# Optimization experiments

Hardware: AMD Instinct MI355X
Metric: run time of the kernel (lower is better)

The kernel has to match this reference:

```python
import jax, jax.numpy as jnp
import numpy as np

N = 50000      # nodes
E = 1600000    # edges
H = 128        # hidden_dim
P = 28         # pocket_dim
G = 256        # graphs in the batch
EPS = 1e-5     # BatchNorm eps


def setup_inputs() -> dict:
    key = jax.random.key(0)
    ks = jax.random.split(key, 24)
    s = 0.05
    inp = {
        "x": jax.random.normal(ks[0], (N, 7), jnp.float32),
        "edge_index": jax.random.randint(ks[1], (2, E), 0, N, jnp.int64),
        "batch": jnp.sort(jax.random.randint(ks[2], (N,), 0, G, jnp.int64)),
        "pocket_features": jax.random.normal(ks[3], (P,), jnp.float32),
        # GCN conv weights (first layer 7->128, layers 2..3 stacked 128->128)
        "conv0_W": jax.random.normal(ks[4], (7, H), jnp.float32) * s,
        "conv0_b": jnp.zeros((H,), jnp.float32),
        "convs_W": jax.random.normal(ks[5], (2, H, H), jnp.float32) * s,
        "convs_b": jnp.zeros((2, H), jnp.float32),
        # BatchNorm (eval mode) params per layer, stacked [3, H]
        "bn_gamma": jnp.ones((3, H), jnp.float32),
        "bn_beta": jnp.zeros((3, H), jnp.float32),
        "bn_mean": jax.random.normal(ks[6], (3, H), jnp.float32) * 0.1,
        "bn_var": jax.random.uniform(ks[7], (3, H), jnp.float32, 0.5, 1.5),
        # pocket MLP 28->64->64
        "pmlp_W1": jax.random.normal(ks[8], (P, 64), jnp.float32) * s,
        "pmlp_b1": jnp.zeros((64,), jnp.float32),
        "pmlp_W2": jax.random.normal(ks[9], (64, 64), jnp.float32) * s,
        "pmlp_b2": jnp.zeros((64,), jnp.float32),
        # Bilinear: torch weight shape [out=64, in1=H, in2=64]
        "bil_W": jax.random.normal(ks[10], (64, H, 64), jnp.float32) * s,
        "bil_b": jnp.zeros((64,), jnp.float32),
        # classifier 64->32->1
        "cls_W1": jax.random.normal(ks[11], (64, 32), jnp.float32) * s,
        "cls_b1": jnp.zeros((32,), jnp.float32),
        "cls_W2": jax.random.normal(ks[12], (32, 1), jnp.float32) * s,
        "cls_b2": jnp.zeros((1,), jnp.float32),
    }
    return inp


def _gcn(x, W, b, src, dst, dinv):
    """PyG GCNConv: sym-normalized aggregation with added self loops."""
    h = x @ W                                  # [N, H']
    norm = dinv[src] * dinv[dst]               # [E]
    agg = jax.ops.segment_sum(norm[:, None] * h[src], dst, num_segments=N)
    agg = agg + (dinv * dinv)[:, None] * h     # self-loop contribution
    return agg + b


def reference(x, edge_index, batch, pocket_features,
              conv0_W, conv0_b, convs_W, convs_b,
              bn_gamma, bn_beta, bn_mean, bn_var,
              pmlp_W1, pmlp_b1, pmlp_W2, pmlp_b2,
              bil_W, bil_b, cls_W1, cls_b1, cls_W2, cls_b2):
    src, dst = edge_index[0], edge_index[1]
    # degree over targets, with +1 for the self loop
    deg = jax.ops.segment_sum(jnp.ones((E,), x.dtype), dst, num_segments=N) + 1.0
    dinv = jax.lax.rsqrt(deg)

    h = x
    for i in range(3):
        W = conv0_W if i == 0 else convs_W[i - 1]
        b = conv0_b if i == 0 else convs_b[i - 1]
        h = _gcn(h, W, b, src, dst, dinv)
        # BatchNorm1d in eval mode; dropout = identity in eval
        h = bn_gamma[i] * (h - bn_mean[i]) * jax.lax.rsqrt(bn_var[i] + EPS) + bn_beta[i]
        h = jax.nn.relu(h)

    # global_mean_pool over graph ids
    sums = jax.ops.segment_sum(h, batch, num_segments=G)              # [G, H]
    cnt = jax.ops.segment_sum(jnp.ones((N,), h.dtype), batch, num_segments=G)
    ligand = sums / jnp.maximum(cnt, 1.0)[:, None]                    # [G, H]

    pk = jax.nn.relu(pocket_features @ pmlp_W1 + pmlp_b1) @ pmlp_W2 + pmlp_b2  # [64]
    pk = jnp.broadcast_to(pk, (G, 64))

    inter = jnp.einsum('bi,oij,bj->bo', ligand, bil_W, pk) + bil_b    # [G, 64]
    z = jax.nn.relu(inter @ cls_W1 + cls_b1) @ cls_W2 + cls_b2        # [G, 1]
    return z[:, 0]
```

## Files before the change

### kernel.cpp

```cpp
#include <hip/hip_runtime.h>

#define EPSBN 1e-5f
#define BCAP 12288
#define OVCAP 262144
#define INS_CAP 24
#define INS_STRIDE 25

#if defined(__has_builtin)
#if __has_builtin(__builtin_amdgcn_cvt_pk_f32_fp8) && __has_builtin(__builtin_amdgcn_cvt_pk_fp8_f32)
#define HAS_CVT_FP8 1
#endif
#endif

typedef float v2f_t __attribute__((ext_vector_type(2)));
typedef __attribute__((ext_vector_type(8))) short bf16x8;
typedef __attribute__((ext_vector_type(4))) float f32x4;

__device__ inline unsigned short f2bf(float f) {
    unsigned int u = __float_as_uint(f);
    u += 0x7fffu + ((u >> 16) & 1u);
    return (unsigned short)(u >> 16);
}

__device__ inline float fp8_dec_byte(int b) {
    int s = (b >> 7) & 1, e = (b >> 3) & 15, m = b & 7;
    float v = (e == 0) ? ldexpf((float)m, -9) : ldexpf((float)(8 + m), e - 10);
    return s ? -v : v;
}
__device__ inline unsigned int fp8_enc(float x) {
    unsigned int u = __float_as_uint(x);
    unsigned int s = u >> 31;
    u &= 0x7fffffffu;
    float a = __uint_as_float(u);
    unsigned int code;
    if (a >= 0.015625f) {
        if (a > 448.0f) code = 0x7E;
        else {
            int exp = (int)(u >> 23) - 127;
            unsigned int mant = u & 0x7fffffu;
            unsigned int keep = mant >> 20;
            unsigned int rest = mant & 0xfffffu;
            code = ((unsigned int)(exp + 7) << 3) | keep;
            unsigned int rnd = (rest > 0x80000u) || (rest == 0x80000u && (code & 1));
            code += rnd;
            if (code > 0x7E) code = 0x7E;
        }
    } else {
        code = (unsigned int)(a * 512.0f + 0.5f);
    }
    return (s << 7) | code;
}

__device__ __forceinline__ void fp8x8_dec(uint2 w, float* v) {
#ifdef HAS_CVT_FP8
    v2f_t l0 = __builtin_amdgcn_cvt_pk_f32_fp8((int)w.x, false);
    v2f_t h0 = __builtin_amdgcn_cvt_pk_f32_fp8((int)w.x, true);
    v2f_t l1 = __builtin_amdgcn_cvt_pk_f32_fp8((int)w.y, false);
    v2f_t h1 = __builtin_amdgcn_cvt_pk_f32_fp8((int)w.y, true);
    v[0] = l0[0]; v[1] = l0[1]; v[2] = h0[0]; v[3] = h0[1];
    v[4] = l1[0]; v[5] = l1[1]; v[6] = h1[0]; v[7] = h1[1];
#else
    v[0] = fp8_dec_byte(w.x & 255);        v[1] = fp8_dec_byte((w.x >> 8) & 255);
    v[2] = fp8_dec_byte((w.x >> 16) & 255); v[3] = fp8_dec_byte(w.x >> 24);
    v[4] = fp8_dec_byte(w.y & 255);        v[5] = fp8_dec_byte((w.y >> 8) & 255);
    v[6] = fp8_dec_byte((w.y >> 16) & 255); v[7] = fp8_dec_byte(w.y >> 24);
#endif
}

__global__ void setup_kernel(int* __restrict__ tails, int ntail,
                             const int* __restrict__ batch, int* __restrict__ gstart,
                             int n, int g,
                             const float* __restrict__ conv0_b, const float* __restrict__ convs_b,
                             const float* __restrict__ gamma, const float* __restrict__ beta,
                             const float* __restrict__ mean, const float* __restrict__ var,
                             float* __restrict__ sc, float* __restrict__ sh,
                             const float* __restrict__ convs_W, unsigned short* __restrict__ Wp,
                             const float* __restrict__ pf, const float* __restrict__ W1,
                             const float* __restrict__ b1, const float* __restrict__ W2,
                             const float* __restrict__ b2, const float* __restrict__ bilW,
                             float* __restrict__ M) {
    int t = threadIdx.x;
    int i = blockIdx.x * 256 + t;
    if (i < ntail * 32) tails[i] = 0;
    if (i < 384) {
        int l = i >> 7, f = i & 127;
        float bias = (l == 0) ? conv0_b[f] : convs_b[(l - 1) * 128 + f];
        float s = gamma[i] * rsqrtf(var[i] + EPSBN);
        sc[i] = s;
        sh[i] = fmaf(s, bias - mean[i], beta[i]);
    }
    if (i < 32768) {
        int l = i >> 14;
        int fidx = i & 16383;
        int j  = fidx & 7;
        int ln = (fidx >> 3) & 63;
        int nt = (fidx >> 9) & 7;
        int kk = fidx >> 12;
        int k = kk * 32 + (ln >> 4) * 8 + j;
        int c = nt * 16 + (ln & 15);
        Wp[i] = f2bf(convs_W[l * 16384 + k * 128 + c]);
    }
    if (i < n) {
        int b = batch[i];
        int bp = (i == 0) ? -1 : batch[i - 1];
        for (int q = bp + 1; q <= b; ++q) gstart[q] = i;
        if (i == n - 1) {
            for (int q = b + 1; q <= g; ++q) gstart[q] = n;
        }
    }
    if (blockIdx.x < 32) {
        __shared__ float h1s[64];
        __shared__ float spk[64];
        if (t < 64) {
            float acc = b1[t];
            #pragma unroll
            for (int k = 0; k < 28; ++k) acc = fmaf(pf[k], W1[k * 64 + t], acc);
            h1s[t] = fmaxf(acc, 0.f);
        }
        __syncthreads();
        if (t < 64) {
            float acc2 = b2[t];
            for (int k = 0; k < 64; ++k) acc2 = fmaf(h1s[k], W2[k * 64 + t], acc2);
            spk[t] = acc2;
        }
        __syncthreads();
        if (i < 64 * 128) {
            const float* wr = bilW + (size_t)i * 64;
            float acc = 0.f;
            #pragma unroll 8
            for (int j = 0; j < 64; ++j) acc = fmaf(wr[j], spk[j], acc);
            M[i] = acc;
        }
    }
}

__launch_bounds__(256)
__global__ void bucket_kernel(const int* __restrict__ src, const int* __restrict__ dst,
                              unsigned int* __restrict__ buckets, int* __restrict__ tails,
                              unsigned int* __restrict__ ovf, int e, int nwq) {
    __shared__ unsigned int buf[256 * INS_STRIDE];
    __shared__ int cnt[256];
    __shared__ int basee[256];
    int t = threadIdx.x;
    cnt[t] = 0;
    __syncthreads();
    int c0 = blockIdx.x * 2048;
    int c1 = min(c0 + 2048, e);
    for (int i = c0 + t; i < c1; i += 256) {
        int d = dst[i];
        int bb = d >> 8;
        unsigned int val = (unsigned int)src[i] | ((unsigned int)d << 16);
        int pos = atomicAdd(&cnt[bb], 1);
        if (pos < INS_CAP) buf[bb * INS_STRIDE + pos] = val;
        else {
            int op = atomicAdd(&tails[nwq * 32], 1);
            if (op < OVCAP) ovf[op] = val;
        }
    }
    __syncthreads();
    int lane = t & 63, wv = t >> 6;
    int bb0 = wv * 64;
    {
        int b = bb0 + lane;
        int c = (b < nwq) ? min(cnt[b], INS_CAP) : 0;
        basee[b] = c ? atomicAdd(&tails[b * 32], c) : 0;
    }
    for (int k = 0; k < 64; ++k) {
        int b = bb0 + k;
        if (b >= nwq) break;
        int c = min(cnt[b], INS_CAP);
        if (c == 0) continue;
        int g = basee[b];
        if (lane < c) {
            unsigned int v = buf[b * INS_STRIDE + lane];
            int gp = g + lane;
            if (gp < BCAP) buckets[(size_t)b * BCAP + gp] = v;
            else {
                int op = atomicAdd(&tails[nwq * 32], 1);
                if (op < OVCAP) ovf[op] = v;
            }
        }
    }
}

__launch_bounds__(256)
__global__ void build_deg(const unsigned int* __restrict__ buckets,
                          const int* __restrict__ tails, const unsigned int* __restrict__ ovf,
                          int* __restrict__ deg, float* __restrict__ dinv,
                          int* __restrict__ winPad, int n, int nwq) {
    __shared__ int degL[256];
    __shared__ int ws4[4];
    int b = blockIdx.x, t = threadIdx.x;
    int lo = b << 8;
    int hi = min(lo + 256, n);
    int nw = hi - lo;
    degL[t] = 0;
    __syncthreads();
    int myvalid = min(tails[b * 32], BCAP);
    const unsigned int* myb = buckets + (size_t)b * BCAP;
    for (int i = t; i < myvalid; i += 256)
        atomicAdd(&degL[(myb[i] >> 16) & 255], 1);
    int ovn = min(tails[nwq * 32], OVCAP);
    for (int i = t; i < ovn; i += 256) {
        unsigned int v = ovf[i];
        int d = v >> 16;
        if (d >= lo && d < hi) atomicAdd(&degL[d & 255], 1);
    }
    __syncthreads();
    int dgi = degL[t];
    if (t < nw) {
        deg[lo + t] = dgi;
        dinv[lo + t] = rsqrtf((float)dgi + 1.0f);
    }
    int pad = (t < nw) ? ((dgi + 15) & ~15) : 0;
    int lane = t & 63, wv = t >> 6;
    int s = pad;
    #pragma unroll
    for (int o = 1; o < 64; o <<= 1) s += __shfl_xor(s, o);
    if (lane == 0) ws4[wv] = s;
    __syncthreads();
    if (t == 0) winPad[b] = ws4[0] + ws4[1] + ws4[2] + ws4[3];
}

__launch_bounds__(256)
__global__ void build_csr2(const unsigned int* __restrict__ buckets,
                           const int* __restrict__ tails, const unsigned int* __restrict__ ovf,
                           const int* __restrict__ deg, const float* __restrict__ dinv,
                           const int* __restrict__ winPad,
                           unsigned int* __restrict__ csr2, int* __restrict__ offs,
                           int n, int nwq) {
    __shared__ int curL[256];
    __shared__ int wsum4[4];
    __shared__ int rsum4[4];
    int b = blockIdx.x, t = threadIdx.x;
    int lo = b << 8;
    int hi = min(lo + 256, n);
    int nw = hi - lo;
    int lane = t & 63, wv = t >> 6;
    int ssum = 0;
    for (int w = t; w < b; w += 256) ssum += winPad[w];
    #pragma unroll
    for (int o = 1; o < 64; o <<= 1) ssum += __shfl_xor(ssum, o);
    if (lane == 0) rsum4[wv] = ssum;
    int mydeg  = (t < nw) ? deg[lo + t] : 0;
    int dpad = (mydeg + 15) & ~15;
    if (t >= nw) dpad = 0;
    int sc0 = dpad;
    #pragma unroll
    for (int o = 1; o < 64; o <<= 1) {
        int u = __shfl_up(sc0, o);
        if (lane >= o) sc0 += u;
    }
    if (lane == 63) wsum4[wv] = sc0;
    __syncthreads();
    int base = rsum4[0] + rsum4[1] + rsum4[2] + rsum4[3];
    int wb = 0;
    for (int q = 0; q < wv; ++q) wb += wsum4[q];
    int myoff = wb + sc0 - dpad;
    curL[t] = myoff;
    int total = wsum4[0] + wsum4[1] + wsum4[2] + wsum4[3];
    for (int q = mydeg; q < dpad; ++q) csr2[base + myoff + q] = 0u;
    __syncthreads();
    int myvalid = min(tails[b * 32], BCAP);
    const unsigned int* myb = buckets + (size_t)b * BCAP;
    for (int i = t; i < myvalid; i += 256) {
        unsigned int v = myb[i];
        int dl = (v >> 16) & 255;
        int s = v & 0xffff;
        int pos = atomicAdd(&curL[dl], 1);
        if (pos < total) {
            unsigned int enc = (unsigned int)f2bf(dinv[s]);
            csr2[base + pos] = (unsigned int)s | (enc << 16);
        }
    }
    int ovn = min(tails[nwq * 32], OVCAP);
    for (int i = t; i < ovn; i += 256) {
        unsigned int v = ovf[i];
        int d = v >> 16;
        if (d >= lo && d < hi) {
            int s = v & 0xffff;
            int pos = atomicAdd(&curL[d & 255], 1);
            if (pos < total) {
                unsigned int enc = (unsigned int)f2bf(dinv[s]);
                csr2[base + pos] = (unsigned int)s | (enc << 16);
            }
        }
    }
    if (t < nw) offs[lo + t] = base + myoff;
}

__device__ __forceinline__ void dense_fp8_out(const unsigned short* hL,
                                              const unsigned short* __restrict__ Wp,
                                              unsigned char* __restrict__ out8,
                                              int b0n, int n, int lane, int wv) {
    f32x4 acc0 = {0.f, 0.f, 0.f, 0.f};
    f32x4 acc1 = {0.f, 0.f, 0.f, 0.f};
    int r = lane & 15, g = lane >> 4;
    int nt0 = wv * 2, nt1 = nt0 + 1;
    #pragma unroll
    for (int kk = 0; kk < 4; ++kk) {
        bf16x8 a  = *(const bf16x8*)(hL + r * 136 + kk * 32 + g * 8);
        bf16x8 b0 = *(const bf16x8*)(Wp + ((kk * 8 + nt0) * 64 + lane) * 8);
        bf16x8 b1 = *(const bf16x8*)(Wp + ((kk * 8 + nt1) * 64 + lane) * 8);
        acc0 = __builtin_amdgcn_mfma_f32_16x16x32_bf16(a, b0, acc0, 0, 0, 0);
        acc1 = __builtin_amdgcn_mfma_f32_16x16x32_bf16(a, b1, acc1, 0, 0, 0);
    }
    #pragma unroll
    for (int j = 0; j < 4; ++j) {
        int node = b0n + g * 4 + j;
        if (node < n) {
            unsigned char q0, q1;
#ifdef HAS_CVT_FP8
            q0 = (unsigned char)(__builtin_amdgcn_cvt_pk_fp8_f32(acc0[j], acc0[j], 0, false) & 0xff);
            q1 = (unsigned char)(__builtin_amdgcn_cvt_pk_fp8_f32(acc1[j], acc1[j], 0, false) & 0xff);
#else
            q0 = (unsigned char)fp8_enc(acc0[j]);
            q1 = (unsigned char)fp8_enc(acc1[j]);
#endif
            out8[(size_t)node * 128 + nt0 * 16 + r] = q0;
            out8[(size_t)node * 128 + nt1 * 16 + r] = q1;
        }
    }
}

__launch_bounds__(256)
__global__ void layer0f_kernel(const float* __restrict__ x, const unsigned int* __restrict__ csr2,
                               const int* __restrict__ offs, const int* __restrict__ degi,
                               const float* __restrict__ dinv, const float* __restrict__ W,
                               const float* __restrict__ sc, const float* __restrict__ sh,
                               const unsigned short* __restrict__ Wp,
                               unsigned char* __restrict__ out8, int n) {
    __shared__ float sW[7 * 128];
    __shared__ float ssc[128], ssh[128];
    __shared__ unsigned short hL[16 * 136];
    int t = threadIdx.x;
    for (int i = t; i < 7 * 128; i += 256) sW[i] = W[i];
    if (t < 128) { ssc[t] = sc[t]; ssh[t] = sh[t]; }
    __syncthreads();
    int lane = t & 63, wv = t >> 6;
    int b0n = blockIdx.x * 16;
    int e = lane >> 3, f = lane & 7;
    for (int nd = 0; nd < 4; ++nd) {
        int node = b0n + wv * 4 + nd;
        bool ok = node < n;
        int off  = ok ? offs[node] : 0;
        int cntp = ok ? ((degi[node] + 15) & ~15) : 0;
        float di = ok ? dinv[node] : 0.f;
        float self = (ok && f < 7) ? x[(size_t)node * 7 + f] : 0.f;
        float acc = 0.f;
        for (int c0 = 0; c0 < cntp; c0 += 16) {
            unsigned int e4[2];
            #pragma unroll
            for (int u = 0; u < 2; ++u) e4[u] = csr2[off + c0 + u * 8 + e];
            float vA[2];
            #pragma unroll
            for (int u = 0; u < 2; ++u) {
                int ss = e4[u] & 0xffff;
                vA[u] = (f < 7) ? x[(size_t)ss * 7 + f] : 0.f;
            }
            #pragma unroll
            for (int u = 0; u < 2; ++u)
                acc = fmaf(__uint_as_float(e4[u] & 0xffff0000u), vA[u], acc);
        }
        if (ok) {
            acc += __shfl_xor(acc, 8);
            acc += __shfl_xor(acc, 16);
            acc += __shfl_xor(acc, 32);
            float xa = di * (acc + di * self);
            float xk[7];
            #pragma unroll
            for (int k = 0; k < 7; ++k) xk[k] = __shfl(xa, k);
            int fo = lane * 2;
            float o0 = 0.f, o1 = 0.f;
            #pragma unroll
            for (int k = 0; k < 7; ++k) {
                o0 = fmaf(xk[k], sW[k * 128 + fo], o0);
                o1 = fmaf(xk[k], sW[k * 128 + fo + 1], o1);
            }
            o0 = fmaxf(fmaf(ssc[fo],     o0, ssh[fo]),     0.f);
            o1 = fmaxf(fmaf(ssc[fo + 1], o1, ssh[fo + 1]), 0.f);
            unsigned int p = (unsigned int)f2bf(o0) | ((unsigned int)f2bf(o1) << 16);
            *(unsigned int*)(&hL[(wv * 4 + nd) * 136 + fo]) = p;
        }
    }
    __syncthreads();
    dense_fp8_out(hL, Wp, out8, b0n, n, lane, wv);
}

template<int DENSE>
__launch_bounds__(256)
__global__ void aggf_kernel(const unsigned int* __restrict__ hw, const unsigned int* __restrict__ csr2,
                            const int* __restrict__ offs, const int* __restrict__ degi,
                            const float* __restrict__ dinv,
                            const float* __restrict__ sc, const float* __restrict__ shv,
                            const unsigned short* __restrict__ Wp,
                            unsigned char* __restrict__ out8,
                            float* __restrict__ outF, int n) {
    __shared__ unsigned short hL[16 * 136];
    int t = threadIdx.x, lane = t & 63, wv = t >> 6;
    int fl = lane & 15, grp = lane >> 4;
    int b0n = blockIdx.x * 16;
    for (int nd = 0; nd < 4; ++nd) {
        int node = b0n + wv * 4 + nd;
        bool ok = node < n;
        int off  = ok ? offs[node] : 0;
        int cntp = ok ? ((degi[node] + 15) & ~15) : 0;
        float di = ok ? dinv[node] : 0.f;
        uint2 ws = ok ? *(const uint2*)(hw + (size_t)node * 32 + fl * 2) : make_uint2(0u, 0u);
        float a[8];
        #pragma unroll
        for (int i = 0; i < 8; ++i) a[i] = 0.f;
        for (int c0 = 0; c0 < cntp; c0 += 16) {
            unsigned int e4[4];
            #pragma unroll
            for (int u = 0; u < 4; ++u) e4[u] = csr2[off + c0 + u * 4 + grp];
            uint2 w[4];
            #pragma unroll
            for (int u = 0; u < 4; ++u) {
                int ss = e4[u] & 0xffff;
                w[u] = *(const uint2*)(hw + (size_t)ss * 32 + fl * 2);
            }
            #pragma unroll
            for (int u = 0; u < 4; ++u) {
                float nn = __uint_as_float(e4[u] & 0xffff0000u);
                float v[8];
                fp8x8_dec(w[u], v);
                #pragma unroll
                for (int i = 0; i < 8; ++i) a[i] = fmaf(nn, v[i], a[i]);
            }
        }
        #pragma unroll
        for (int i = 0; i < 8; ++i) {
            a[i] += __shfl_xor(a[i], 16);
            a[i] += __shfl_xor(a[i], 32);
        }
        if (grp == 0 && ok) {
            float sv[8];
            fp8x8_dec(ws, sv);
            int f0 = fl * 8;
            float vo[8];
            #pragma unroll
            for (int i = 0; i < 8; ++i) {
                float vv = (a[i] + di * sv[i]) * di;
                vo[i] = fmaxf(fmaf(sc[f0 + i], vv, shv[f0 + i]), 0.f);
            }
            if (DENSE) {
                uint4 P;
                P.x = (unsigned int)f2bf(vo[0]) | ((unsigned int)f2bf(vo[1]) << 16);
                P.y = (unsigned int)f2bf(vo[2]) | ((unsigned int)f2bf(vo[3]) << 16);
                P.z = (unsigned int)f2bf(vo[4]) | ((unsigned int)f2bf(vo[5]) << 16);
                P.w = (unsigned int)f2bf(vo[6]) | ((unsigned int)f2bf(vo[7]) << 16);
                *(uint4*)(&hL[(wv * 4 + nd) * 136 + f0]) = P;
            } else {
                float4 o0 = make_float4(vo[0], vo[1], vo[2], vo[3]);
                float4 o1 = make_float4(vo[4], vo[5], vo[6], vo[7]);
                *(float4*)(outF + (size_t)node * 128 + f0)     = o0;
                *(float4*)(outF + (size_t)node * 128 + f0 + 4) = o1;
            }
        }
    }
    if (DENSE) {
        __syncthreads();
        dense_fp8_out(hL, Wp, out8, b0n, n, lane, wv);
    }
}

__launch_bounds__(128)
__global__ void final_kernel(const float* __restrict__ h, const int* __restrict__ gstart,
                             const float* __restrict__ M, const float* __restrict__ bil_b,
                             const float* __restrict__ cW1, const float* __restrict__ cb1,
                             const float* __restrict__ cW2, const float* __restrict__ cb2,
                             float* __restrict__ out) {
    __shared__ float lig[128];
    __shared__ float inter[64];
    __shared__ float hc[32];
    int g = blockIdx.x, t = threadIdx.x;
    int s = gstart[g], e = gstart[g + 1];
    float a[8];
    #pragma unroll
    for (int q = 0; q < 8; ++q) a[q] = 0.f;
    int i = s;
    for (; i + 8 <= e; i += 8) {
        #pragma unroll
        for (int q = 0; q < 8; ++q)
            a[q] += h[(size_t)(i + q) * 128 + t];
    }
    for (; i < e; ++i) a[0] += h[(size_t)i * 128 + t];
    float c = (float)(e - s); if (c < 1.f) c = 1.f;
    lig[t] = (((a[0] + a[1]) + (a[2] + a[3])) + ((a[4] + a[5]) + (a[6] + a[7]))) / c;
    __syncthreads();
    if (t < 64) {
        float acc = bil_b[t];
        const float* mr = M + (size_t)t * 128;
        #pragma unroll 8
        for (int k = 0; k < 128; ++k) acc = fmaf(lig[k], mr[k], acc);
        inter[t] = acc;
    }
    __syncthreads();
    if (t < 32) {
        float acc = cb1[t];
        #pragma unroll 8
        for (int o = 0; o < 64; ++o) acc = fmaf(inter[o], cW1[o * 32 + t], acc);
        hc[t] = fmaxf(acc, 0.f);
    }
    __syncthreads();
    if (t == 0) {
        float acc = cb2[0];
        #pragma unroll
        for (int j = 0; j < 32; ++j) acc = fmaf(hc[j], cW2[j], acc);
        out[g] = acc;
    }
}

extern "C" void kernel_launch(void* const* d_in, const int* in_sizes, int n_in,
                              void* d_out, int out_size, void* d_ws, size_t ws_size,
                              hipStream_t stream) {
    const float* x        = (const float*)d_in[0];
    const int*   edge     = (const int*)d_in[1];
    const int*   batch    = (const int*)d_in[2];
    const float* pocket   = (const float*)d_in[3];
    const float* conv0_W  = (const float*)d_in[4];
    const float* conv0_b  = (const float*)d_in[5];
    const float* convs_W  = (const float*)d_in[6];
    const float* convs_b  = (const float*)d_in[7];
    const float* bn_gamma = (const float*)d_in[8];
    const float* bn_beta  = (const float*)d_in[9];
    const float* bn_mean  = (const float*)d_in[10];
    const float* bn_var   = (const float*)d_in[11];
    const float* pmlp_W1  = (const float*)d_in[12];
    const float* pmlp_b1  = (const float*)d_in[13];
    const float* pmlp_W2  = (const float*)d_in[14];
    const float* pmlp_b2  = (const float*)d_in[15];
    const float* bil_W    = (const float*)d_in[16];
    const float* bil_b    = (const float*)d_in[17];
    const float* cls_W1   = (const float*)d_in[18];
    const float* cls_b1   = (const float*)d_in[19];
    const float* cls_W2   = (const float*)d_in[20];
    const float* cls_b2   = (const float*)d_in[21];

    const int N = in_sizes[0] / 7;
    const int E = in_sizes[1] / 2;
    const int G = out_size;
    const int* srcA = edge;
    const int* dstA = edge + E;
    const int NB  = (N + 255) / 256;
    const int NWQ = (N + 255) >> 8;
    const int NBL = (N + 15) / 16;

    char* p = (char*)d_ws;
    auto alloc = [&](size_t bytes) -> void* {
        void* r = (void*)p;
        p += (bytes + 255) & ~(size_t)255;
        return r;
    };
    int*   tails    = (int*)alloc((size_t)(NWQ + 1) * 32 * 4);
    unsigned int* buckets = (unsigned int*)alloc((size_t)NWQ * BCAP * 4);
    unsigned int* ovf     = (unsigned int*)alloc((size_t)OVCAP * 4);
    int*   deg      = (int*)alloc((size_t)N * 4);
    int*   offs     = (int*)alloc((size_t)N * 4);
    float* dinv     = (float*)alloc((size_t)N * 4);
    int*   winPad   = (int*)alloc((size_t)NWQ * 4);
    unsigned int* csr2 = (unsigned int*)alloc(((size_t)E + 15 * (size_t)N + 4096) * 4);
    unsigned char* bufH8a = (unsigned char*)alloc((size_t)N * 128);
    unsigned char* bufH8b = (unsigned char*)alloc((size_t)N * 128);
    float* bufF     = (float*)alloc((size_t)N * 128 * 4);
    int*   gstart   = (int*)alloc((size_t)(G + 1) * 4);
    float* M        = (float*)alloc(64 * 128 * 4);
    float* sc       = (float*)alloc(384 * 4);
    float* shv      = (float*)alloc(384 * 4);
    unsigned short* Wp = (unsigned short*)alloc((size_t)2 * 16384 * 2);

    setup_kernel<<<NB, 256, 0, stream>>>(tails, NWQ + 1, batch, gstart, N, G,
                                         conv0_b, convs_b, bn_gamma, bn_beta, bn_mean, bn_var,
                                         sc, shv, convs_W, Wp,
                                         pocket, pmlp_W1, pmlp_b1, pmlp_W2, pmlp_b2, bil_W, M);
    bucket_kernel<<<(E + 2047) / 2048, 256, 0, stream>>>(srcA, dstA, buckets, tails, ovf,
                                                         E, NWQ);
    build_deg<<<NWQ, 256, 0, stream>>>(buckets, tails, ovf, deg, dinv, winPad, N, NWQ);
    build_csr2<<<NWQ, 256, 0, stream>>>(buckets, tails, ovf, deg, dinv, winPad,
                                        csr2, offs, N, NWQ);

    layer0f_kernel<<<NBL, 256, 0, stream>>>(x, csr2, offs, deg, dinv, conv0_W,
                                            sc, shv, Wp, bufH8a, N);
    aggf_kernel<1><<<NBL, 256, 0, stream>>>((const unsigned int*)bufH8a, csr2, offs, deg, dinv,
                                            sc + 128, shv + 128, Wp + 16384, bufH8b, nullptr, N);
    aggf_kernel<0><<<NBL, 256, 0, stream>>>((const unsigned int*)bufH8b, csr2, offs, deg, dinv,
                                            sc + 256, shv + 256, nullptr, nullptr, bufF, N);

    final_kernel<<<G, 128, 0, stream>>>(bufF, gstart, M, bil_b, cls_W1, cls_b1, cls_W2, cls_b2,
                                        (float*)d_out);
}
```

Before: 293.5 us.

## Fuse degree and CSR build with grid barrier, prefetch edges, widen final pool

Merges build_deg and build_csr2 into a single kernel that uses a software grid-wide barrier (atomic counter plus spin) so the padded window sums and dinv are visible before CSR fill, saving a launch and re-reads of bucket data. Adds one-chunk-ahead software prefetch of CSR edge words in layer0 and the aggregation kernels, and hoists per-node offset/degree/dinv loads. The final pooling kernel now uses 256 threads splitting rows across two halves. The spin barrier assumes all NWQ blocks are co-resident, which risks deadlock if occupancy is insufficient, and it relies on the barrier counter slot in tails having been zeroed by setup.

```diff
diff --git a/kernel.cpp b/kernel.cpp
--- a/kernel.cpp
+++ b/kernel.cpp
@@ -184,16 +184,20 @@
 }
 
 __launch_bounds__(256)
-__global__ void build_deg(const unsigned int* __restrict__ buckets,
-                          const int* __restrict__ tails, const unsigned int* __restrict__ ovf,
+__global__ void build_all(const unsigned int* __restrict__ buckets,
+                          int* __restrict__ tails, const unsigned int* __restrict__ ovf,
                           int* __restrict__ deg, float* __restrict__ dinv,
-                          int* __restrict__ winPad, int n, int nwq) {
+                          int* __restrict__ winPad,
+                          unsigned int* __restrict__ csr2, int* __restrict__ offs,
+                          int n, int nwq) {
     __shared__ int degL[256];
-    __shared__ int ws4[4];
+    __shared__ int curL[256];
+    __shared__ int ws4[4], wsum4[4], rsum4[4];
     int b = blockIdx.x, t = threadIdx.x;
     int lo = b << 8;
     int hi = min(lo + 256, n);
     int nw = hi - lo;
+    int lane = t & 63, wv = t >> 6;
     degL[t] = 0;
     __syncthreads();
     int myvalid = min(tails[b * 32], BCAP);
@@ -212,39 +216,29 @@
         deg[lo + t] = dgi;
         dinv[lo + t] = rsqrtf((float)dgi + 1.0f);
     }
-    int pad = (t < nw) ? ((dgi + 15) & ~15) : 0;
-    int lane = t & 63, wv = t >> 6;
-    int s = pad;
-    #pragma unroll
-    for (int o = 1; o < 64; o <<= 1) s += __shfl_xor(s, o);
-    if (lane == 0) ws4[wv] = s;
+    int dpad = (t < nw) ? ((dgi + 15) & ~15) : 0;
+    {
+        int s = dpad;
+        #pragma unroll
+        for (int o = 1; o < 64; o <<= 1) s += __shfl_xor(s, o);
+        if (lane == 0) ws4[wv] = s;
+    }
     __syncthreads();
     if (t == 0) winPad[b] = ws4[0] + ws4[1] + ws4[2] + ws4[3];
-}
-
-__launch_bounds__(256)
-__global__ void build_csr2(const unsigned int* __restrict__ buckets,
-                           const int* __restrict__ tails, const unsigned int* __restrict__ ovf,
-                           const int* __restrict__ deg, const float* __restrict__ dinv,
-                           const int* __restrict__ winPad,
-                           unsigned int* __restrict__ csr2, int* __restrict__ offs,
-                           int n, int nwq) {
-    __shared__ int curL[256];
-    __shared__ int wsum4[4];
-    __shared__ int rsum4[4];
-    int b = blockIdx.x, t = threadIdx.x;
-    int lo = b << 8;
-    int hi = min(lo + 256, n);
-    int nw = hi - lo;
-    int lane = t & 63, wv = t >> 6;
+    __threadfence();
+    __syncthreads();
+    if (t == 0) {
+        atomicAdd(&tails[nwq * 32 + 8], 1);
+        volatile int* syncp = tails + nwq * 32 + 8;
+        while (*syncp < nwq) { __builtin_amdgcn_s_sleep(2); }
+    }
+    __syncthreads();
+    __threadfence();
     int ssum = 0;
     for (int w = t; w < b; w += 256) ssum += winPad[w];
     #pragma unroll
     for (int o = 1; o < 64; o <<= 1) ssum += __shfl_xor(ssum, o);
     if (lane == 0) rsum4[wv] = ssum;
-    int mydeg  = (t < nw) ? deg[lo + t] : 0;
-    int dpad = (mydeg + 15) & ~15;
-    if (t >= nw) dpad = 0;
     int sc0 = dpad;
     #pragma unroll
     for (int o = 1; o < 64; o <<= 1) {
@@ -259,21 +253,19 @@
     int myoff = wb + sc0 - dpad;
     curL[t] = myoff;
     int total = wsum4[0] + wsum4[1] + wsum4[2] + wsum4[3];
-    for (int q = mydeg; q < dpad; ++q) csr2[base + myoff + q] = 0u;
-    __syncthreads();
-    int myvalid = min(tails[b * 32], BCAP);
-    const unsigned int* myb = buckets + (size_t)b * BCAP;
+    for (int q = dgi; q < dpad; ++q) csr2[base + myoff + q] = 0u;
+    __syncthreads();
+    volatile const float* dvv = (volatile const float*)dinv;
     for (int i = t; i < myvalid; i += 256) {
         unsigned int v = myb[i];
         int dl = (v >> 16) & 255;
         int s = v & 0xffff;
         int pos = atomicAdd(&curL[dl], 1);
         if (pos < total) {
-            unsigned int enc = (unsigned int)f2bf(dinv[s]);
+            unsigned int enc = (unsigned int)f2bf(dvv[s]);
             csr2[base + pos] = (unsigned int)s | (enc << 16);
         }
     }
-    int ovn = min(tails[nwq * 32], OVCAP);
     for (int i = t; i < ovn; i += 256) {
         unsigned int v = ovf[i];
         int d = v >> 16;
@@ -281,7 +273,7 @@
             int s = v & 0xffff;
             int pos = atomicAdd(&curL[d & 255], 1);
             if (pos < total) {
-                unsigned int enc = (unsigned int)f2bf(dinv[s]);
+                unsigned int enc = (unsigned int)f2bf(dvv[s]);
                 csr2[base + pos] = (unsigned int)s | (enc << 16);
             }
         }
@@ -348,10 +340,18 @@
         float di = ok ? dinv[node] : 0.f;
         float self = (ok && f < 7) ? x[(size_t)node * 7 + f] : 0.f;
         float acc = 0.f;
+        unsigned int e4n[2];
+        if (cntp > 0) {
+            #pragma unroll
+            for (int u = 0; u < 2; ++u) e4n[u] = csr2[off + u * 8 + e];
+        }
         for (int c0 = 0; c0 < cntp; c0 += 16) {
             unsigned int e4[2];
             #pragma unroll
-            for (int u = 0; u < 2; ++u) e4[u] = csr2[off + c0 + u * 8 + e];
+            for (int u = 0; u < 2; ++u) e4[u] = e4n[u];
+            int c1 = (c0 + 16 < cntp) ? c0 + 16 : c0;
+            #pragma unroll
+            for (int u = 0; u < 2; ++u) e4n[u] = csr2[off + c1 + u * 8 + e];
             float vA[2];
             #pragma unroll
             for (int u = 0; u < 2; ++u) {
@@ -400,20 +400,36 @@
     int t = threadIdx.x, lane = t & 63, wv = t >> 6;
     int fl = lane & 15, grp = lane >> 4;
     int b0n = blockIdx.x * 16;
+    int offv[4], cntv[4]; float divv[4];
+    #pragma unroll
     for (int nd = 0; nd < 4; ++nd) {
         int node = b0n + wv * 4 + nd;
         bool ok = node < n;
-        int off  = ok ? offs[node] : 0;
-        int cntp = ok ? ((degi[node] + 15) & ~15) : 0;
-        float di = ok ? dinv[node] : 0.f;
+        offv[nd] = ok ? offs[node] : 0;
+        cntv[nd] = ok ? ((degi[node] + 15) & ~15) : 0;
+        divv[nd] = ok ? dinv[node] : 0.f;
+    }
+    for (int nd = 0; nd < 4; ++nd) {
+        int node = b0n + wv * 4 + nd;
+        bool ok = node < n;
+        int off = offv[nd], cntp = cntv[nd];
+        float di = divv[nd];
         uint2 ws = ok ? *(const uint2*)(hw + (size_t)node * 32 + fl * 2) : make_uint2(0u, 0u);
         float a[8];
         #pragma unroll
         for (int i = 0; i < 8; ++i) a[i] = 0.f;
+        unsigned int e4n[4];
+        if (cntp > 0) {
+            #pragma unroll
+            for (int u = 0; u < 4; ++u) e4n[u] = csr2[off + u * 4 + grp];
+        }
         for (int c0 = 0; c0 < cntp; c0 += 16) {
             unsigned int e4[4];
             #pragma unroll
-            for (int u = 0; u < 4; ++u) e4[u] = csr2[off + c0 + u * 4 + grp];
+            for (int u = 0; u < 4; ++u) e4[u] = e4n[u];
+            int c1 = (c0 + 16 < cntp) ? c0 + 16 : c0;
+            #pragma unroll
+            for (int u = 0; u < 4; ++u) e4n[u] = csr2[off + c1 + u * 4 + grp];
             uint2 w[4];
             #pragma unroll
             for (int u = 0; u < 4; ++u) {
@@ -465,35 +481,39 @@
     }
 }
 
-__launch_bounds__(128)
+__launch_bounds__(256)
 __global__ void final_kernel(const float* __restrict__ h, const int* __restrict__ gstart,
                              const float* __restrict__ M, const float* __restrict__ bil_b,
                              const float* __restrict__ cW1, const float* __restrict__ cb1,
                              const float* __restrict__ cW2, const float* __restrict__ cb2,
                              float* __restrict__ out) {
-    __shared__ float lig[128];
+    __shared__ float lig2[2][128];
     __shared__ float inter[64];
     __shared__ float hc[32];
     int g = blockIdx.x, t = threadIdx.x;
+    int half = t >> 7, tid = t & 127;
     int s = gstart[g], e = gstart[g + 1];
-    float a[8];
-    #pragma unroll
-    for (int q = 0; q < 8; ++q) a[q] = 0.f;
-    int i = s;
-    for (; i + 8 <= e; i += 8) {
-        #pragma unroll
-        for (int q = 0; q < 8; ++q)
-            a[q] += h[(size_t)(i + q) * 128 + t];
-    }
-    for (; i < e; ++i) a[0] += h[(size_t)i * 128 + t];
-    float c = (float)(e - s); if (c < 1.f) c = 1.f;
-    lig[t] = (((a[0] + a[1]) + (a[2] + a[3])) + ((a[4] + a[5]) + (a[6] + a[7]))) / c;
+    float a0 = 0.f, a1 = 0.f, a2 = 0.f, a3 = 0.f;
+    int i = s + half;
+    for (; i + 6 < e; i += 8) {
+        a0 += h[(size_t)(i + 0) * 128 + tid];
+        a1 += h[(size_t)(i + 2) * 128 + tid];
+        a2 += h[(size_t)(i + 4) * 128 + tid];
+        a3 += h[(size_t)(i + 6) * 128 + tid];
+    }
+    for (; i < e; i += 2) a0 += h[(size_t)i * 128 + tid];
+    lig2[half][tid] = (a0 + a1) + (a2 + a3);
+    __syncthreads();
+    if (t < 128) {
+        float c = (float)(e - s); if (c < 1.f) c = 1.f;
+        lig2[0][t] = (lig2[0][t] + lig2[1][t]) / c;
+    }
     __syncthreads();
     if (t < 64) {
         float acc = bil_b[t];
         const float* mr = M + (size_t)t * 128;
         #pragma unroll 8
-        for (int k = 0; k < 128; ++k) acc = fmaf(lig[k], mr[k], acc);
+        for (int k = 0; k < 128; ++k) acc = fmaf(lig2[0][k], mr[k], acc);
         inter[t] = acc;
     }
     __syncthreads();
@@ -576,9 +596,8 @@
                                          pocket, pmlp_W1, pmlp_b1, pmlp_W2, pmlp_b2, bil_W, M);
     bucket_kernel<<<(E + 2047) / 2048, 256, 0, stream>>>(srcA, dstA, buckets, tails, ovf,
                                                          E, NWQ);
-    build_deg<<<NWQ, 256, 0, stream>>>(buckets, tails, ovf, deg, dinv, winPad, N, NWQ);
-    build_csr2<<<NWQ, 256, 0, stream>>>(buckets, tails, ovf, deg, dinv, winPad,
-                                        csr2, offs, N, NWQ);
+    build_all<<<NWQ, 256, 0, stream>>>(buckets, tails, ovf, deg, dinv, winPad,
+                                       csr2, offs, N, NWQ);
 
     layer0f_kernel<<<NBL, 256, 0, stream>>>(x, csr2, offs, deg, dinv, conv0_W,
                                             sc, shv, Wp, bufH8a, N);
@@ -587,6 +606,6 @@
     aggf_kernel<0><<<NBL, 256, 0, stream>>>((const unsigned int*)bufH8b, csr2, offs, deg, dinv,
                                             sc + 256, shv + 256, nullptr, nullptr, bufF, N);
 
-    final_kernel<<<G, 128, 0, stream>>>(bufF, gstart, M, bil_b, cls_W1, cls_b1, cls_W2, cls_b2,
+    final_kernel<<<G, 256, 0, stream>>>(bufF, gstart, M, bil_b, cls_W1, cls_b1, cls_W2, cls_b2,
                                         (float*)d_out);
 }
```

Result: slower. 311.6 us (+6.2%).
